# Kernel optimization log

Hardware: AMD Instinct MI355X
Metric: run time of the kernel (lower is better)

The kernel has to match this reference:

```python
import jax, jax.numpy as jnp
import numpy as np

ALPHA = 0.2
NEG_BIG = -9e15


def setup_inputs() -> dict:
    key = jax.random.key(0)
    k1, k2, k3, k4 = jax.random.split(key, 4)
    N, F_in, F_out = 8192, 512, 128
    h = jax.random.normal(k1, (N, F_in), dtype=jnp.float32)
    adj = jax.random.randint(k2, (N, N), 0, 2, dtype=jnp.int32)
    W = jax.random.normal(k3, (F_in, F_out), dtype=jnp.float32) * 0.05
    a = jax.random.normal(k4, (2 * F_out, 1), dtype=jnp.float32) * 0.05
    return {"h": h, "adj": adj, "W": W, "a": a}


def reference(h, adj, W, a):
    F_out = W.shape[1]
    Wh = h @ W                                  # [N, F_out]
    Wh1 = Wh @ a[:F_out, :]                     # [N, 1]
    Wh2 = Wh @ a[F_out:, :]                     # [N, 1]
    e = Wh1 + Wh2.T                             # [N, N] broadcast add
    e = jnp.where(e >= 0, e, ALPHA * e)         # LeakyReLU
    scores = jnp.where(adj > 0, e, NEG_BIG)     # adjacency mask
    attention = jax.nn.softmax(scores, axis=1)  # row-wise softmax
    h_prime = attention @ Wh                    # [N, F_out]
    return jax.nn.elu(h_prime)                  # concat=True -> elu
```

## Files before the change

### kernel.cpp

```cpp
#include <hip/hip_runtime.h>
#include <stdint.h>

typedef float f32x4 __attribute__((ext_vector_type(4)));
typedef __bf16 bf16x8 __attribute__((ext_vector_type(8)));
typedef unsigned short u16;
typedef unsigned int u32;

#define N_NODES 8192
#define F_IN 512
#define F_OUT 128
#define LRA 0.2f

__device__ __forceinline__ u16 f32_to_bf16(float f) {
  union { float f; u32 u; } v; v.f = f;
  u32 u = v.u;
  u += 0x7fffu + ((u >> 16) & 1u);
  return (u16)(u >> 16);
}
__device__ __forceinline__ float bf16_to_f32(u16 h) {
  union { u32 u; float f; } v; v.u = ((u32)h) << 16;
  return v.f;
}

__global__ __launch_bounds__(256) void gemm_wh(
    const float* __restrict__ h, const float* __restrict__ W,
    const float* __restrict__ av,
    u16* __restrict__ WhT, float* __restrict__ Wh1, float* __restrict__ Wh2) {
  __shared__ float At[32][36];
  __shared__ float Bs[32][132];
  const int t = threadIdx.x;
  const int i0 = blockIdx.x * 32;
  const int tm = t >> 5, tn = t & 31;
  const int lrow = t >> 3, lc = t & 7;

  f32x4 acc[4];
#pragma unroll
  for (int r = 0; r < 4; ++r) acc[r] = (f32x4){0.f, 0.f, 0.f, 0.f};

  for (int kc = 0; kc < F_IN; kc += 32) {
    f32x4 a4 = *(const f32x4*)&h[(size_t)(i0 + lrow) * F_IN + kc + lc * 4];
    At[lc * 4 + 0][lrow] = a4[0];
    At[lc * 4 + 1][lrow] = a4[1];
    At[lc * 4 + 2][lrow] = a4[2];
    At[lc * 4 + 3][lrow] = a4[3];
#pragma unroll
    for (int q = 0; q < 4; ++q) {
      int c = (lc + q * 8) * 4;
      *(f32x4*)&Bs[lrow][c] = *(const f32x4*)&W[(size_t)(kc + lrow) * F_OUT + c];
    }
    __syncthreads();
#pragma unroll
    for (int k = 0; k < 32; ++k) {
      f32x4 b4 = *(f32x4*)&Bs[k][tn * 4];
      f32x4 a4k = *(f32x4*)&At[k][tm * 4];
#pragma unroll
      for (int r = 0; r < 4; ++r) acc[r] += b4 * a4k[r];
    }
    __syncthreads();
  }

#pragma unroll
  for (int r = 0; r < 4; ++r) *(f32x4*)&Bs[tm * 4 + r][tn * 4] = acc[r];
  __syncthreads();

  {
    const int d = t >> 1, ih = (t & 1) * 16;
    u32 u[8];
#pragma unroll
    for (int e = 0; e < 8; ++e) {
      u32 lo = f32_to_bf16(Bs[ih + 2 * e][d]);
      u32 hi = f32_to_bf16(Bs[ih + 2 * e + 1][d]);
      u[e] = lo | (hi << 16);
    }
    u32* dst = (u32*)&WhT[(size_t)d * N_NODES + i0 + ih];
    uint4 v0; v0.x = u[0]; v0.y = u[1]; v0.z = u[2]; v0.w = u[3];
    uint4 v1; v1.x = u[4]; v1.y = u[5]; v1.z = u[6]; v1.w = u[7];
    *(uint4*)dst = v0;
    *(uint4*)(dst + 4) = v1;
  }

  {
    const int w = t >> 6, l = t & 63;
#pragma unroll
    for (int rr = 0; rr < 8; ++rr) {
      int row = w * 8 + rr;
      float x0 = Bs[row][l], x1 = Bs[row][l + 64];
      float s1 = x0 * av[l] + x1 * av[l + 64];
      float s2 = x0 * av[128 + l] + x1 * av[192 + l];
#pragma unroll
      for (int m = 32; m >= 1; m >>= 1) {
        s1 += __shfl_xor(s1, m, 64);
        s2 += __shfl_xor(s2, m, 64);
      }
      if (l == 0) { Wh1[i0 + row] = s1; Wh2[i0 + row] = s2; }
    }
  }
}

__global__ __launch_bounds__(256) void gat_main(
    const int* __restrict__ adj, const float* __restrict__ Wh1,
    const float* __restrict__ Wh2, const u16* __restrict__ WhT,
    float* __restrict__ accp, float* __restrict__ sp,
    const int js, const int jlen) {
  __shared__ u16 Plds[64][72];
  __shared__ u16 Vlds[128][72];
  __shared__ float sscr[256];

  const int t = threadIdx.x;
  const int bi = (int)blockIdx.x / js;
  const int jsi = (int)blockIdx.x % js;
  const int i0 = bi * 64;
  const int j0 = jsi * jlen;

  const int vd = t >> 1, vh = (t & 1) * 32;
  const int il = t >> 2, q4 = (t & 3) * 16;
  const float cI = Wh1[i0 + il];
  const int w = t >> 6, l = t & 63, r = l & 15, oct = l >> 4;

  f32x4 acc[4][2];
#pragma unroll
  for (int it = 0; it < 4; ++it)
#pragma unroll
    for (int dt = 0; dt < 2; ++dt) acc[it][dt] = (f32x4){0.f, 0.f, 0.f, 0.f};
  float sAcc = 0.f;

  for (int ch = 0; ch < jlen; ch += 64) {
    const int jc = j0 + ch;

#pragma unroll
    for (int q = 0; q < 4; ++q) {
      uint4 v = *(const uint4*)&WhT[(size_t)vd * N_NODES + jc + vh + q * 8];
      *(uint4*)&Vlds[vd][vh + q * 8] = v;
    }

    const int* arow = &adj[(size_t)(i0 + il) * N_NODES + jc + q4];
    const float* w2p = &Wh2[jc + q4];
#pragma unroll
    for (int k = 0; k < 4; ++k) {
      int4 a4 = *(const int4*)&arow[k * 4];
      f32x4 w2 = *(const f32x4*)&w2p[k * 4];
      int ai[4] = {a4.x, a4.y, a4.z, a4.w};
      u16 pu[4];
#pragma unroll
      for (int e = 0; e < 4; ++e) {
        float x = cI + w2[e];
        x = x >= 0.f ? x : LRA * x;
        float p = __expf(x);
        p = ai[e] ? p : 0.f;
        u16 b = f32_to_bf16(p);
        pu[e] = b;
        sAcc += bf16_to_f32(b);
      }
      ushort4 pv; pv.x = pu[0]; pv.y = pu[1]; pv.z = pu[2]; pv.w = pu[3];
      *(ushort4*)&Plds[il][q4 + k * 4] = pv;
    }
    __syncthreads();

#pragma unroll
    for (int ks = 0; ks < 2; ++ks) {
      const int col = ks * 32 + oct * 8;
      bf16x8 b0 = *(bf16x8*)&Vlds[w * 32 + r][col];
      bf16x8 b1 = *(bf16x8*)&Vlds[w * 32 + 16 + r][col];
#pragma unroll
      for (int it = 0; it < 4; ++it) {
        bf16x8 af = *(bf16x8*)&Plds[it * 16 + r][col];
        acc[it][0] = __builtin_amdgcn_mfma_f32_16x16x32_bf16(af, b0, acc[it][0], 0, 0, 0);
        acc[it][1] = __builtin_amdgcn_mfma_f32_16x16x32_bf16(af, b1, acc[it][1], 0, 0, 0);
      }
    }
    __syncthreads();
  }

  sscr[t] = sAcc;
  __syncthreads();
  if (t < 64) {
    float s = sscr[4 * t] + sscr[4 * t + 1] + sscr[4 * t + 2] + sscr[4 * t + 3];
    sp[(size_t)jsi * N_NODES + i0 + t] = s;
  }

#pragma unroll
  for (int it = 0; it < 4; ++it) {
#pragma unroll
    for (int dt = 0; dt < 2; ++dt) {
#pragma unroll
      for (int rr = 0; rr < 4; ++rr) {
        int row = i0 + it * 16 + oct * 4 + rr;
        int dcol = w * 32 + dt * 16 + r;
        accp[((size_t)jsi * N_NODES + row) * F_OUT + dcol] = acc[it][dt][rr];
      }
    }
  }
}

__global__ __launch_bounds__(256) void finalize_k(
    const float* __restrict__ accp, const float* __restrict__ sp,
    float* __restrict__ out, const int js) {
  const int idx = blockIdx.x * 256 + threadIdx.x;
  const int i = idx >> 7;
  float num = 0.f, den = 0.f;
  for (int s = 0; s < js; ++s) {
    num += accp[(size_t)s * (N_NODES * F_OUT) + idx];
    den += sp[(size_t)s * N_NODES + i];
  }
  float x = num / den;
  out[idx] = x > 0.f ? x : expm1f(x);
}

extern "C" void kernel_launch(void* const* d_in, const int* in_sizes, int n_in,
                              void* d_out, int out_size, void* d_ws, size_t ws_size,
                              hipStream_t stream) {
  const float* h = (const float*)d_in[0];
  const int* adj = (const int*)d_in[1];
  const float* W = (const float*)d_in[2];
  const float* av = (const float*)d_in[3];
  float* out = (float*)d_out;
  char* ws = (char*)d_ws;

  u16* WhT = (u16*)ws;
  float* Wh1 = (float*)(ws + (2ull << 20));
  float* Wh2 = (float*)(ws + (2ull << 20) + (32ull << 10));
  float* sp = (float*)(ws + (2ull << 20) + (64ull << 10));
  float* accp = (float*)(ws + (2ull << 20) + (320ull << 10));
  const size_t base = (2ull << 20) + (320ull << 10);

  int js = 8;
  while (js > 1 && base + (size_t)js * N_NODES * F_OUT * 4 > ws_size) js >>= 1;
  const int jlen = N_NODES / js;

  gemm_wh<<<N_NODES / 32, 256, 0, stream>>>(h, W, av, WhT, Wh1, Wh2);
  gat_main<<<(N_NODES / 64) * js, 256, 0, stream>>>(adj, Wh1, Wh2, WhT, accp, sp, js, jlen);
  finalize_k<<<(N_NODES * F_OUT) / 256, 256, 0, stream>>>(accp, sp, out, js);
}
```

Before: 120.5 us.

## Use bf16 MFMA for Wh GEMM with prepacked W, double-buffer attention P tiles

Result: faster. 113.3 us (-6.0%).

```diff
diff --git a/kernel.cpp b/kernel.cpp
--- a/kernel.cpp
+++ b/kernel.cpp
@@ -21,79 +21,144 @@
   union { u32 u; float f; } v; v.u = ((u32)h) << 16;
   return v.f;
 }
+__device__ __forceinline__ float dot4(f32x4 a, f32x4 b) {
+  return a[0] * b[0] + a[1] * b[1] + a[2] * b[2] + a[3] * b[3];
+}
+
+__global__ __launch_bounds__(256) void prep_k(
+    const float* __restrict__ W, const float* __restrict__ av,
+    u16* __restrict__ WT, float* __restrict__ wa) {
+  __shared__ u16 Ts[F_OUT][40];
+  const int t = threadIdx.x, kc = (int)blockIdx.x * 32;
+  {
+    const int k = t >> 3, dof = (t & 7) * 16;
+#pragma unroll
+    for (int q = 0; q < 4; ++q) {
+      f32x4 v = *(const f32x4*)&W[(size_t)(kc + k) * F_OUT + dof + q * 4];
+#pragma unroll
+      for (int e = 0; e < 4; ++e) Ts[dof + q * 4 + e][k] = f32_to_bf16(v[e]);
+    }
+  }
+  __syncthreads();
+  {
+    const int d = t >> 1, kh = (t & 1) * 16;
+    uint4 o0 = *(uint4*)&Ts[d][kh];
+    uint4 o1 = *(uint4*)&Ts[d][kh + 8];
+    *(uint4*)&WT[(size_t)d * F_IN + kc + kh] = o0;
+    *(uint4*)&WT[(size_t)d * F_IN + kc + kh + 8] = o1;
+  }
+  {
+    const int kl = t >> 3, l8 = t & 7;
+    const float* wrow = &W[(size_t)(kc + kl) * F_OUT];
+    float s1 = 0.f, s2 = 0.f;
+#pragma unroll
+    for (int q = 0; q < 2; ++q) {
+      int dd = l8 * 16 + q * 8;
+      f32x4 w0 = *(const f32x4*)&wrow[dd];
+      f32x4 w1 = *(const f32x4*)&wrow[dd + 4];
+      s1 += dot4(w0, *(const f32x4*)&av[dd]) + dot4(w1, *(const f32x4*)&av[dd + 4]);
+      s2 += dot4(w0, *(const f32x4*)&av[F_OUT + dd]) + dot4(w1, *(const f32x4*)&av[F_OUT + dd + 4]);
+    }
+#pragma unroll
+    for (int m = 1; m <= 4; m <<= 1) {
+      s1 += __shfl_xor(s1, m, 64);
+      s2 += __shfl_xor(s2, m, 64);
+    }
+    if (l8 == 0) { wa[kc + kl] = s1; wa[F_IN + kc + kl] = s2; }
+  }
+}
 
 __global__ __launch_bounds__(256) void gemm_wh(
-    const float* __restrict__ h, const float* __restrict__ W,
-    const float* __restrict__ av,
+    const float* __restrict__ h, const u16* __restrict__ WT,
+    const float* __restrict__ wa,
     u16* __restrict__ WhT, float* __restrict__ Wh1, float* __restrict__ Wh2) {
-  __shared__ float At[32][36];
-  __shared__ float Bs[32][132];
+  __shared__ u16 Ab[2][32][80];
+  __shared__ u16 Bs[2][F_OUT][80];
   const int t = threadIdx.x;
-  const int i0 = blockIdx.x * 32;
-  const int tm = t >> 5, tn = t & 31;
-  const int lrow = t >> 3, lc = t & 7;
+  const int i0 = (int)blockIdx.x * 32;
+  const int w = t >> 6, l = t & 63, r = l & 15, oct = l >> 4;
+  const int mrow = (w & 1) * 16, ncol = (w >> 1) * 64;
+  const int ar = t >> 3, ak = (t & 7) * 8;
+  const int br = t >> 1, bk = (t & 1) * 32;
+
+  const float* hrow = &h[(size_t)(i0 + ar) * F_IN + ak];
+  const u16* wtrow = &WT[(size_t)br * F_IN + bk];
+  const float* wap = &wa[ak];
+  const float* wbp = &wa[F_IN + ak];
 
   f32x4 acc[4];
 #pragma unroll
-  for (int r = 0; r < 4; ++r) acc[r] = (f32x4){0.f, 0.f, 0.f, 0.f};
-
-  for (int kc = 0; kc < F_IN; kc += 32) {
-    f32x4 a4 = *(const f32x4*)&h[(size_t)(i0 + lrow) * F_IN + kc + lc * 4];
-    At[lc * 4 + 0][lrow] = a4[0];
-    At[lc * 4 + 1][lrow] = a4[1];
-    At[lc * 4 + 2][lrow] = a4[2];
-    At[lc * 4 + 3][lrow] = a4[3];
-#pragma unroll
-    for (int q = 0; q < 4; ++q) {
-      int c = (lc + q * 8) * 4;
-      *(f32x4*)&Bs[lrow][c] = *(const f32x4*)&W[(size_t)(kc + lrow) * F_OUT + c];
-    }
-    __syncthreads();
-#pragma unroll
-    for (int k = 0; k < 32; ++k) {
-      f32x4 b4 = *(f32x4*)&Bs[k][tn * 4];
-      f32x4 a4k = *(f32x4*)&At[k][tm * 4];
-#pragma unroll
-      for (int r = 0; r < 4; ++r) acc[r] += b4 * a4k[r];
-    }
-    __syncthreads();
-  }
-
-#pragma unroll
-  for (int r = 0; r < 4; ++r) *(f32x4*)&Bs[tm * 4 + r][tn * 4] = acc[r];
+  for (int nf = 0; nf < 4; ++nf) acc[nf] = (f32x4){0.f, 0.f, 0.f, 0.f};
+  float s1 = 0.f, s2 = 0.f;
+
+  f32x4 ra0, ra1;
+  uint4 rb[4];
+
+#define STORE_A(B)                                                        \
+  { u32 p0 = f32_to_bf16(ra0[0]) | ((u32)f32_to_bf16(ra0[1]) << 16);      \
+    u32 p1 = f32_to_bf16(ra0[2]) | ((u32)f32_to_bf16(ra0[3]) << 16);      \
+    u32 p2 = f32_to_bf16(ra1[0]) | ((u32)f32_to_bf16(ra1[1]) << 16);      \
+    u32 p3 = f32_to_bf16(ra1[2]) | ((u32)f32_to_bf16(ra1[3]) << 16);      \
+    uint4 v; v.x = p0; v.y = p1; v.z = p2; v.w = p3;                      \
+    *(uint4*)&Ab[B][ar][ak] = v; }
+#define STORE_B(B)                                                        \
+  { *(uint4*)&Bs[B][br][bk + 0]  = rb[0];                                 \
+    *(uint4*)&Bs[B][br][bk + 8]  = rb[1];                                 \
+    *(uint4*)&Bs[B][br][bk + 16] = rb[2];                                 \
+    *(uint4*)&Bs[B][br][bk + 24] = rb[3]; }
+
+  ra0 = *(const f32x4*)&hrow[0];
+  ra1 = *(const f32x4*)&hrow[4];
+#pragma unroll
+  for (int j = 0; j < 4; ++j) rb[j] = *(const uint4*)&wtrow[j * 8];
+  s1 += dot4(ra0, *(const f32x4*)&wap[0]) + dot4(ra1, *(const f32x4*)&wap[4]);
+  s2 += dot4(ra0, *(const f32x4*)&wbp[0]) + dot4(ra1, *(const f32x4*)&wbp[4]);
+  STORE_A(0); STORE_B(0);
   __syncthreads();
 
-  {
-    const int d = t >> 1, ih = (t & 1) * 16;
-    u32 u[8];
-#pragma unroll
-    for (int e = 0; e < 8; ++e) {
-      u32 lo = f32_to_bf16(Bs[ih + 2 * e][d]);
-      u32 hi = f32_to_bf16(Bs[ih + 2 * e + 1][d]);
-      u[e] = lo | (hi << 16);
-    }
-    u32* dst = (u32*)&WhT[(size_t)d * N_NODES + i0 + ih];
-    uint4 v0; v0.x = u[0]; v0.y = u[1]; v0.z = u[2]; v0.w = u[3];
-    uint4 v1; v1.x = u[4]; v1.y = u[5]; v1.z = u[6]; v1.w = u[7];
-    *(uint4*)dst = v0;
-    *(uint4*)(dst + 4) = v1;
-  }
-
-  {
-    const int w = t >> 6, l = t & 63;
-#pragma unroll
-    for (int rr = 0; rr < 8; ++rr) {
-      int row = w * 8 + rr;
-      float x0 = Bs[row][l], x1 = Bs[row][l + 64];
-      float s1 = x0 * av[l] + x1 * av[l + 64];
-      float s2 = x0 * av[128 + l] + x1 * av[192 + l];
-#pragma unroll
-      for (int m = 32; m >= 1; m >>= 1) {
-        s1 += __shfl_xor(s1, m, 64);
-        s2 += __shfl_xor(s2, m, 64);
+#pragma unroll
+  for (int it = 0; it < 8; ++it) {
+    const int buf = it & 1;
+    if (it < 7) {
+      const int kc = (it + 1) * 64;
+      ra0 = *(const f32x4*)&hrow[kc];
+      ra1 = *(const f32x4*)&hrow[kc + 4];
+#pragma unroll
+      for (int j = 0; j < 4; ++j) rb[j] = *(const uint4*)&wtrow[kc + j * 8];
+      s1 += dot4(ra0, *(const f32x4*)&wap[kc]) + dot4(ra1, *(const f32x4*)&wap[kc + 4]);
+      s2 += dot4(ra0, *(const f32x4*)&wbp[kc]) + dot4(ra1, *(const f32x4*)&wbp[kc + 4]);
+    }
+#pragma unroll
+    for (int ks = 0; ks < 2; ++ks) {
+      bf16x8 af = *(bf16x8*)&Ab[buf][mrow + r][ks * 32 + oct * 8];
+#pragma unroll
+      for (int nf = 0; nf < 4; ++nf) {
+        bf16x8 bfv = *(bf16x8*)&Bs[buf][ncol + nf * 16 + r][ks * 32 + oct * 8];
+        acc[nf] = __builtin_amdgcn_mfma_f32_16x16x32_bf16(af, bfv, acc[nf], 0, 0, 0);
       }
-      if (l == 0) { Wh1[i0 + row] = s1; Wh2[i0 + row] = s2; }
-    }
+    }
+    if (it < 7) {
+      STORE_A(buf ^ 1); STORE_B(buf ^ 1);
+      __syncthreads();
+    }
+  }
+#undef STORE_A
+#undef STORE_B
+
+#pragma unroll
+  for (int m = 1; m <= 4; m <<= 1) {
+    s1 += __shfl_xor(s1, m, 64);
+    s2 += __shfl_xor(s2, m, 64);
+  }
+  if ((t & 7) == 0) { Wh1[i0 + ar] = s1; Wh2[i0 + ar] = s2; }
+
+#pragma unroll
+  for (int nf = 0; nf < 4; ++nf) {
+    u32 lo = f32_to_bf16(acc[nf][0]) | ((u32)f32_to_bf16(acc[nf][1]) << 16);
+    u32 hi = f32_to_bf16(acc[nf][2]) | ((u32)f32_to_bf16(acc[nf][3]) << 16);
+    const int d = ncol + nf * 16 + r;
+    uint2 v; v.x = lo; v.y = hi;
+    *(uint2*)&WhT[(size_t)d * N_NODES + i0 + mrow + oct * 4] = v;
   }
 }
 
@@ -102,8 +167,7 @@
     const float* __restrict__ Wh2, const u16* __restrict__ WhT,
     float* __restrict__ accp, float* __restrict__ sp,
     const int js, const int jlen) {
-  __shared__ u16 Plds[64][72];
-  __shared__ u16 Vlds[128][72];
+  __shared__ u16 Plds[2][64][80];
   __shared__ float sscr[256];
 
   const int t = threadIdx.x;
@@ -112,11 +176,13 @@
   const int i0 = bi * 64;
   const int j0 = jsi * jlen;
 
-  const int vd = t >> 1, vh = (t & 1) * 32;
   const int il = t >> 2, q4 = (t & 3) * 16;
   const float cI = Wh1[i0 + il];
   const int w = t >> 6, l = t & 63, r = l & 15, oct = l >> 4;
 
+  const u16* vp0 = &WhT[(size_t)(w * 32 + r) * N_NODES];
+  const u16* vp1 = &WhT[(size_t)(w * 32 + 16 + r) * N_NODES];
+
   f32x4 acc[4][2];
 #pragma unroll
   for (int it = 0; it < 4; ++it)
@@ -126,12 +192,12 @@
 
   for (int ch = 0; ch < jlen; ch += 64) {
     const int jc = j0 + ch;
-
-#pragma unroll
-    for (int q = 0; q < 4; ++q) {
-      uint4 v = *(const uint4*)&WhT[(size_t)vd * N_NODES + jc + vh + q * 8];
-      *(uint4*)&Vlds[vd][vh + q * 8] = v;
-    }
+    const int buf = (ch >> 6) & 1;
+
+    bf16x8 b00 = *(const bf16x8*)&vp0[jc + oct * 8];
+    bf16x8 b01 = *(const bf16x8*)&vp0[jc + 32 + oct * 8];
+    bf16x8 b10 = *(const bf16x8*)&vp1[jc + oct * 8];
+    bf16x8 b11 = *(const bf16x8*)&vp1[jc + 32 + oct * 8];
 
     const int* arow = &adj[(size_t)(i0 + il) * N_NODES + jc + q4];
     const float* w2p = &Wh2[jc + q4];
@@ -152,23 +218,21 @@
         sAcc += bf16_to_f32(b);
       }
       ushort4 pv; pv.x = pu[0]; pv.y = pu[1]; pv.z = pu[2]; pv.w = pu[3];
-      *(ushort4*)&Plds[il][q4 + k * 4] = pv;
+      *(ushort4*)&Plds[buf][il][q4 + k * 4] = pv;
     }
     __syncthreads();
 
 #pragma unroll
     for (int ks = 0; ks < 2; ++ks) {
-      const int col = ks * 32 + oct * 8;
-      bf16x8 b0 = *(bf16x8*)&Vlds[w * 32 + r][col];
-      bf16x8 b1 = *(bf16x8*)&Vlds[w * 32 + 16 + r][col];
+      bf16x8 bA = ks ? b01 : b00;
+      bf16x8 bB = ks ? b11 : b10;
 #pragma unroll
       for (int it = 0; it < 4; ++it) {
-        bf16x8 af = *(bf16x8*)&Plds[it * 16 + r][col];
-        acc[it][0] = __builtin_amdgcn_mfma_f32_16x16x32_bf16(af, b0, acc[it][0], 0, 0, 0);
-        acc[it][1] = __builtin_amdgcn_mfma_f32_16x16x32_bf16(af, b1, acc[it][1], 0, 0, 0);
+        bf16x8 af = *(bf16x8*)&Plds[buf][it * 16 + r][ks * 32 + oct * 8];
+        acc[it][0] = __builtin_amdgcn_mfma_f32_16x16x32_bf16(af, bA, acc[it][0], 0, 0, 0);
+        acc[it][1] = __builtin_amdgcn_mfma_f32_16x16x32_bf16(af, bB, acc[it][1], 0, 0, 0);
       }
     }
-    __syncthreads();
   }
 
   sscr[t] = sAcc;
@@ -195,7 +259,7 @@
 __global__ __launch_bounds__(256) void finalize_k(
     const float* __restrict__ accp, const float* __restrict__ sp,
     float* __restrict__ out, const int js) {
-  const int idx = blockIdx.x * 256 + threadIdx.x;
+  const int idx = (int)blockIdx.x * 256 + threadIdx.x;
   const int i = idx >> 7;
   float num = 0.f, den = 0.f;
   for (int s = 0; s < js; ++s) {
@@ -216,18 +280,21 @@
   float* out = (float*)d_out;
   char* ws = (char*)d_ws;
 
-  u16* WhT = (u16*)ws;
-  float* Wh1 = (float*)(ws + (2ull << 20));
-  float* Wh2 = (float*)(ws + (2ull << 20) + (32ull << 10));
-  float* sp = (float*)(ws + (2ull << 20) + (64ull << 10));
-  float* accp = (float*)(ws + (2ull << 20) + (320ull << 10));
-  const size_t base = (2ull << 20) + (320ull << 10);
+  u16* WT = (u16*)ws;
+  float* wa = (float*)(ws + (256ull << 10));
+  u16* WhT = (u16*)(ws + (512ull << 10));
+  float* Wh1 = (float*)(ws + (512ull << 10) + (2ull << 20));
+  float* Wh2 = (float*)(ws + (512ull << 10) + (2ull << 20) + (32ull << 10));
+  float* sp = (float*)(ws + (512ull << 10) + (2ull << 20) + (64ull << 10));
+  float* accp = (float*)(ws + (512ull << 10) + (2ull << 20) + (320ull << 10));
+  const size_t base = (512ull << 10) + (2ull << 20) + (320ull << 10);
 
   int js = 8;
   while (js > 1 && base + (size_t)js * N_NODES * F_OUT * 4 > ws_size) js >>= 1;
   const int jlen = N_NODES / js;
 
-  gemm_wh<<<N_NODES / 32, 256, 0, stream>>>(h, W, av, WhT, Wh1, Wh2);
+  prep_k<<<16, 256, 0, stream>>>(W, av, WT, wa);
+  gemm_wh<<<N_NODES / 32, 256, 0, stream>>>(h, WT, wa, WhT, Wh1, Wh2);
   gat_main<<<(N_NODES / 64) * js, 256, 0, stream>>>(adj, Wh1, Wh2, WhT, accp, sp, js, jlen);
   finalize_k<<<(N_NODES * F_OUT) / 256, 256, 0, stream>>>(accp, sp, out, js);
 }
```
